# Kernel optimization log

Hardware: AMD Instinct MI355X
Metric: run time of the kernel (lower is better)

Reference implementation:

```python
import jax, jax.numpy as jnp
import numpy as np
from jax import lax

B, T, D = 64, 1024, 256   # batch, seq_len, input_size
H, C = 1024, 1000         # hidden_size, num_classes


def setup_inputs() -> dict:
    key = jax.random.key(0)
    k_x, k_ih, k_hh, k_b, k_fc, k_fb = jax.random.split(key, 6)
    x = jax.random.normal(k_x, (B, T, D), dtype=jnp.float32)
    # scaled init so the 1024-step recurrence stays numerically sane
    w_ih = jax.random.normal(k_ih, (H, D), dtype=jnp.float32) * (1.0 / np.sqrt(D))
    w_hh = jax.random.normal(k_hh, (H, H), dtype=jnp.float32) * (0.5 / np.sqrt(H))
    b_mod = jax.random.normal(k_b, (H,), dtype=jnp.float32) * 0.01 - 0.1
    w_fc = jax.random.normal(k_fc, (C, H), dtype=jnp.float32) * (1.0 / np.sqrt(H))
    b_fc = jnp.zeros((C,), dtype=jnp.float32)
    return {"x": x, "w_ih": w_ih, "w_hh": w_hh, "b_mod": b_mod,
            "w_fc": w_fc, "b_fc": b_fc}


def reference(x, w_ih, w_hh, b_mod, w_fc, b_fc):
    # modReLU RNN: h_t = sign(z_t) * relu(|z_t| + b),  z_t = W_ih x_t + W_hh h_{t-1}
    # fc head applied to last hidden state (out[:, -1, :]).
    bsz = x.shape[0]
    # precompute input projections for all timesteps: [B, T, H]
    xproj = jnp.einsum('btd,hd->bth', x, w_ih)

    def step(h, x_t):
        z = x_t + h @ w_hh.T                      # [B, H]
        h_new = jnp.sign(z) * jnp.maximum(jnp.abs(z) + b_mod, 0.0)
        return h_new, None

    h0 = jnp.zeros((bsz, w_hh.shape[0]), dtype=x.dtype)
    h_last, _ = lax.scan(step, h0, jnp.swapaxes(xproj, 0, 1))  # scan over T
    return h_last @ w_fc.T + b_fc  # [B, C]
```

## Files before the change

### kernel.cpp

```cpp
#include <hip/hip_runtime.h>

typedef __bf16 bf16;
typedef __bf16 bf16x4 __attribute__((ext_vector_type(4)));
typedef __bf16 bf16x8 __attribute__((ext_vector_type(8)));
typedef float f32x4 __attribute__((ext_vector_type(4)));
typedef int   i32x4 __attribute__((ext_vector_type(4)));
typedef unsigned long long u64;
typedef unsigned int u32;

#define T_STEPS 1024
#define BATCH   64
#define DIN     256
#define HID     1024
#define NBLK    32
#define RING    8
#define SENT    0x7F7F7F7Fu

__global__ __launch_bounds__(256) void xproj_gemm(
    const float* __restrict__ x, const float* __restrict__ w_ih,
    bf16* __restrict__ xproj)
{
    __shared__ bf16 As[128 * 40];
    __shared__ bf16 Bs[128 * 40];
    const int tid = threadIdx.x;
    const int m0 = blockIdx.x * 128;
    const int n0 = blockIdx.y * 128;
    const int w = tid >> 6, lane = tid & 63;
    const int r = lane & 15, q = lane >> 4;

    f32x4 acc[2][8];
    #pragma unroll
    for (int i = 0; i < 2; i++)
        #pragma unroll
        for (int j = 0; j < 8; j++)
            acc[i][j] = (f32x4){0.f, 0.f, 0.f, 0.f};

    for (int kk = 0; kk < 8; kk++) {
        const int k0 = kk * 32;
        __syncthreads();
        #pragma unroll
        for (int j = 0; j < 4; j++) {
            int u = tid + j * 256;
            int row = u >> 3, c4 = u & 7;
            float4 fa = *(const float4*)&x[(size_t)(m0 + row) * DIN + k0 + c4 * 4];
            bf16x4 va = { (bf16)fa.x, (bf16)fa.y, (bf16)fa.z, (bf16)fa.w };
            *(bf16x4*)&As[row * 40 + c4 * 4] = va;
            float4 fb = *(const float4*)&w_ih[(size_t)(n0 + row) * DIN + k0 + c4 * 4];
            bf16x4 vb = { (bf16)fb.x, (bf16)fb.y, (bf16)fb.z, (bf16)fb.w };
            *(bf16x4*)&Bs[row * 40 + c4 * 4] = vb;
        }
        __syncthreads();
        bf16x8 a0 = *(const bf16x8*)&As[(w * 32 + r) * 40 + q * 8];
        bf16x8 a1 = *(const bf16x8*)&As[(w * 32 + 16 + r) * 40 + q * 8];
        #pragma unroll
        for (int nt = 0; nt < 8; nt++) {
            bf16x8 bb = *(const bf16x8*)&Bs[(nt * 16 + r) * 40 + q * 8];
            acc[0][nt] = __builtin_amdgcn_mfma_f32_16x16x32_bf16(a0, bb, acc[0][nt], 0, 0, 0);
            acc[1][nt] = __builtin_amdgcn_mfma_f32_16x16x32_bf16(a1, bb, acc[1][nt], 0, 0, 0);
        }
    }

    #pragma unroll
    for (int mi = 0; mi < 2; mi++)
        #pragma unroll
        for (int nt = 0; nt < 8; nt++)
            #pragma unroll
            for (int reg = 0; reg < 4; reg++) {
                int gm = m0 + w * 32 + mi * 16 + q * 4 + reg;
                int n  = n0 + nt * 16 + r;
                int b  = gm >> 10, t = gm & 1023;
                xproj[(((t << 6) + b) << 10) + n] = (bf16)acc[mi][nt][reg];
            }
}

__global__ __launch_bounds__(512, 2) void rnn_rec(
    const float* __restrict__ w_hh, const float* __restrict__ b_mod,
    const bf16* __restrict__ xproj, u64* __restrict__ hbuf,
    float* __restrict__ hT)
{
    __shared__ bf16 Wl[64 * 1032];
    __shared__ float Red[24 * 272];

    const int tid = threadIdx.x;
    const int fg2 = (int)(blockIdx.x >> 1);
    const int half = (int)(blockIdx.x & 1);
    const int f0 = fg2 * 64;
    const int b0 = half * 32;
    const int w = tid >> 6, lane = tid & 63;
    const int r = lane & 15, q = lane >> 4;
    const int bg = w & 1, kq = w >> 1;
    const int batchA = b0 + bg * 16 + r;

    for (int j = 0; j < 32; j++) {
        int u = tid + j * 512;
        int row = u >> 8, c4 = u & 255;
        float4 f = *(const float4*)&w_hh[(size_t)(f0 + row) * HID + c4 * 4];
        bf16x4 v = { (bf16)f.x, (bf16)f.y, (bf16)f.z, (bf16)f.w };
        *(bf16x4*)&Wl[row * 1032 + c4 * 4] = v;
    }
    const int myF = f0 + kq * 16 + r;
    const float bc = b_mod[myF];
    __syncthreads();

    bf16x8 Bf[4][8];
    #pragma unroll
    for (int nt = 0; nt < 4; nt++)
        #pragma unroll
        for (int ks = 0; ks < 8; ks++)
            Bf[nt][ks] = *(const bf16x8*)&Wl[(nt * 16 + r) * 1032 + kq * 256 + ks * 32 + q * 8];

    u32* hbuf32 = (u32*)hbuf;
    const size_t fragOff = (size_t)batchA * 2048 + kq * 512 + q * 16;

    float xpv[4];
    #pragma unroll
    for (int reg = 0; reg < 4; reg++) {
        int b = b0 + bg * 16 + q * 4 + reg;
        xpv[reg] = (float)xproj[(b << 10) + myF];
    }

    for (int t = 0; t < T_STEPS; t++) {
        const int rp = t & (RING - 1), wp = (t + 1) & (RING - 1);
        const char* Hb = (const char*)hbuf + (size_t)rp * 131072 + fragOff;

        union { i32x4 v[8]; u32 wd[32]; bf16x8 f[8]; } A;
        for (;;) {
            asm volatile(
                "global_load_dwordx4 %0, %8, off sc0 sc1\n\t"
                "global_load_dwordx4 %1, %8, off offset:64 sc0 sc1\n\t"
                "global_load_dwordx4 %2, %8, off offset:128 sc0 sc1\n\t"
                "global_load_dwordx4 %3, %8, off offset:192 sc0 sc1\n\t"
                "global_load_dwordx4 %4, %8, off offset:256 sc0 sc1\n\t"
                "global_load_dwordx4 %5, %8, off offset:320 sc0 sc1\n\t"
                "global_load_dwordx4 %6, %8, off offset:384 sc0 sc1\n\t"
                "global_load_dwordx4 %7, %8, off offset:448 sc0 sc1\n\t"
                "s_waitcnt vmcnt(0)"
                : "=v"(A.v[0]), "=v"(A.v[1]), "=v"(A.v[2]), "=v"(A.v[3]),
                  "=v"(A.v[4]), "=v"(A.v[5]), "=v"(A.v[6]), "=v"(A.v[7])
                : "v"(Hb)
                : "memory");
            bool ok = true;
            #pragma unroll
            for (int i = 0; i < 32; i++) ok &= (A.wd[i] != SENT);
            if (__all((int)ok)) break;
        }

        f32x4 acc[4];
        #pragma unroll
        for (int nt = 0; nt < 4; nt++) acc[nt] = (f32x4){0.f,0.f,0.f,0.f};
        #pragma unroll
        for (int ks = 0; ks < 8; ks++)
            #pragma unroll
            for (int nt = 0; nt < 4; nt++)
                acc[nt] = __builtin_amdgcn_mfma_f32_16x16x32_bf16(A.f[ks], Bf[nt][ks], acc[nt], 0, 0, 0);

        #pragma unroll
        for (int nt = 0; nt < 4; nt++) {
            if (nt == kq) continue;
            const int s = (kq - nt - 1) & 3;
            const int base = ((bg * 4 + nt) * 3 + s) * 272;
            #pragma unroll
            for (int reg = 0; reg < 4; reg++)
                Red[base + (q * 4 + reg) * 17 + r] = acc[nt][reg];
        }
        __syncthreads();

        float hv4[4];
        #pragma unroll
        for (int reg = 0; reg < 4; reg++) {
            float z = acc[kq][reg];
            #pragma unroll
            for (int s = 0; s < 3; s++)
                z += Red[((bg * 4 + kq) * 3 + s) * 272 + (q * 4 + reg) * 17 + r];
            z += xpv[reg];
            hv4[reg] = copysignf(fmaxf(fabsf(z) + bc, 0.0f), z);
        }
        __syncthreads();

        if (t == T_STEPS - 1) {
            #pragma unroll
            for (int reg = 0; reg < 4; reg++)
                hT[myF * 64 + b0 + bg * 16 + q * 4 + reg] = hv4[reg];
        } else {
            #pragma unroll
            for (int reg = 0; reg < 4; reg++) {
                const int b = b0 + bg * 16 + q * 4 + reg;
                float other = __shfl_xor(hv4[reg], 1);
                if ((r & 1) == 0) {
                    u32 lo = (u32)__builtin_bit_cast(unsigned short, (bf16)hv4[reg]);
                    u32 hi = (u32)__builtin_bit_cast(unsigned short, (bf16)other);
                    __hip_atomic_store(&hbuf32[(size_t)wp * 32768 + (b << 9) + (myF >> 1)],
                                       lo | (hi << 16), __ATOMIC_RELAXED, __HIP_MEMORY_SCOPE_AGENT);
                }
            }
            const size_t sp = (size_t)((t + 4) & (RING - 1)) * 32768;
            #pragma unroll
            for (int reg = 0; reg < 4; reg++) {
                const int b = b0 + bg * 16 + q * 4 + reg;
                if ((r & 1) == 0)
                    __hip_atomic_store(&hbuf32[sp + (b << 9) + (myF >> 1)],
                                       SENT, __ATOMIC_RELAXED, __HIP_MEMORY_SCOPE_AGENT);
            }
            #pragma unroll
            for (int reg = 0; reg < 4; reg++) {
                int b = b0 + bg * 16 + q * 4 + reg;
                xpv[reg] = (float)xproj[((size_t)(t + 1) << 16) + (b << 10) + myF];
            }
        }
    }
}

__global__ __launch_bounds__(256) void fc_head(
    const float* __restrict__ hT, const float* __restrict__ w_fc,
    const float* __restrict__ b_fc, float* __restrict__ out)
{
    const int tid = threadIdx.x;
    const int b = tid & 63;
    const int c = blockIdx.x * 4 + (tid >> 6);
    float acc = b_fc[c];
    #pragma unroll 8
    for (int k = 0; k < HID; k++)
        acc = fmaf(hT[k * 64 + b], w_fc[(size_t)c * HID + k], acc);
    out[b * 1000 + c] = acc;
}

extern "C" void kernel_launch(void* const* d_in, const int* in_sizes, int n_in,
                              void* d_out, int out_size, void* d_ws, size_t ws_size,
                              hipStream_t stream)
{
    const float* x     = (const float*)d_in[0];
    const float* w_ih  = (const float*)d_in[1];
    const float* w_hh  = (const float*)d_in[2];
    const float* b_mod = (const float*)d_in[3];
    const float* w_fc  = (const float*)d_in[4];
    const float* b_fc  = (const float*)d_in[5];
    float* out = (float*)d_out;

    char* ws = (char*)d_ws;
    bf16*  xproj = (bf16*)ws;
    u64*   hbuf  = (u64*)(ws + 134217728);
    float* hT    = (float*)(ws + 134217728 + 1048576);

    hipMemsetAsync(hbuf, 0, 131072, stream);
    hipMemsetAsync((char*)hbuf + 131072, 0x7F, 7 * 131072, stream);

    dim3 g1(512, 8);
    xproj_gemm<<<g1, 256, 0, stream>>>(x, w_ih, xproj);
    rnn_rec<<<NBLK, 512, 0, stream>>>(w_hh, b_mod, xproj, hbuf, hT);
    fc_head<<<250, 256, 0, stream>>>(hT, w_fc, b_fc, out);
}
```

Baseline: 5.019 ms.

## Restructure recurrence into 16 blocks with software-pipelined prefetched h polling

The recurrent kernel now runs 16 blocks of 256 threads. Each block owns 64 hidden features and processes all 64 batch rows as four 16-row sub-steps, where the old kernel split each feature group across two blocks by batch half. The hidden-state fragment for the next sub-step is loaded with relaxed atomic loads into a double buffer while the current sub-step computes, so the spin-wait on the ring buffer overlaps with MFMA work. The aim is to hide global-memory poll latency and cut cross-block synchronization. The cost is four serialized sub-steps per timestep in each block, fewer CUs in use, and a __syncthreads per sub-step.

```diff
diff --git a/kernel.cpp b/kernel.cpp
--- a/kernel.cpp
+++ b/kernel.cpp
@@ -4,16 +4,15 @@
 typedef __bf16 bf16x4 __attribute__((ext_vector_type(4)));
 typedef __bf16 bf16x8 __attribute__((ext_vector_type(8)));
 typedef float f32x4 __attribute__((ext_vector_type(4)));
-typedef int   i32x4 __attribute__((ext_vector_type(4)));
 typedef unsigned long long u64;
+typedef u64 u64x2 __attribute__((ext_vector_type(2)));
 typedef unsigned int u32;
 
 #define T_STEPS 1024
 #define BATCH   64
 #define DIN     256
 #define HID     1024
-#define NBLK    32
-#define RING    8
+#define NFB     16
 #define SENT    0x7F7F7F7Fu
 
 __global__ __launch_bounds__(256) void xproj_gemm(
@@ -73,26 +72,46 @@
             }
 }
 
-__global__ __launch_bounds__(512, 2) void rnn_rec(
+__device__ __forceinline__ void poll_issue(u64* dst, const u64* src)
+{
+    #pragma unroll
+    for (int j = 0; j < 8; j++) {
+        dst[2 * j]     = __hip_atomic_load(src + (size_t)j * 8,
+                                           __ATOMIC_RELAXED, __HIP_MEMORY_SCOPE_AGENT);
+        dst[2 * j + 1] = __hip_atomic_load(src + (size_t)j * 8 + 1,
+                                           __ATOMIC_RELAXED, __HIP_MEMORY_SCOPE_AGENT);
+    }
+    __builtin_amdgcn_sched_barrier(0);
+}
+
+__device__ __forceinline__ int poll_clean(const u64* b)
+{
+    int ok = 1;
+    #pragma unroll
+    for (int j = 0; j < 16; j++) {
+        u64 v = b[j];
+        ok &= ((u32)v != SENT);
+        ok &= ((u32)(v >> 32) != SENT);
+    }
+    return __all(ok);
+}
+
+__global__ __launch_bounds__(256, 1) void rnn_rec(
     const float* __restrict__ w_hh, const float* __restrict__ b_mod,
     const bf16* __restrict__ xproj, u64* __restrict__ hbuf,
     float* __restrict__ hT)
 {
     __shared__ bf16 Wl[64 * 1032];
-    __shared__ float Red[24 * 272];
-
-    const int tid = threadIdx.x;
-    const int fg2 = (int)(blockIdx.x >> 1);
-    const int half = (int)(blockIdx.x & 1);
-    const int f0 = fg2 * 64;
-    const int b0 = half * 32;
-    const int w = tid >> 6, lane = tid & 63;
+    __shared__ f32x4 Red[2][12][64];
+
+    const int tid  = threadIdx.x;
+    const int f0   = (int)blockIdx.x * 64;
+    const int kq   = tid >> 6;
+    const int lane = tid & 63;
     const int r = lane & 15, q = lane >> 4;
-    const int bg = w & 1, kq = w >> 1;
-    const int batchA = b0 + bg * 16 + r;
-
-    for (int j = 0; j < 32; j++) {
-        int u = tid + j * 512;
+
+    for (int j = 0; j < 64; j++) {
+        int u = tid + j * 256;
         int row = u >> 8, c4 = u & 255;
         float4 f = *(const float4*)&w_hh[(size_t)(f0 + row) * HID + c4 * 4];
         bf16x4 v = { (bf16)f.x, (bf16)f.y, (bf16)f.z, (bf16)f.w };
@@ -110,101 +129,91 @@
             Bf[nt][ks] = *(const bf16x8*)&Wl[(nt * 16 + r) * 1032 + kq * 256 + ks * 32 + q * 8];
 
     u32* hbuf32 = (u32*)hbuf;
-    const size_t fragOff = (size_t)batchA * 2048 + kq * 512 + q * 16;
-
-    float xpv[4];
-    #pragma unroll
-    for (int reg = 0; reg < 4; reg++) {
-        int b = b0 + bg * 16 + q * 4 + reg;
-        xpv[reg] = (float)xproj[(b << 10) + myF];
-    }
+    const int fragU = r * 256 + kq * 64 + q * 2;
+
+    float xpv[4][4];
+    #pragma unroll
+    for (int s = 0; s < 4; s++)
+        #pragma unroll
+        for (int reg = 0; reg < 4; reg++)
+            xpv[s][reg] = (float)xproj[((s * 16 + q * 4 + reg) << 10) + myF];
+
+    u64 pb[2][16];
+    poll_issue(pb[0], hbuf + 0 * 4096 + fragU);
+    poll_issue(pb[1], hbuf + 1 * 4096 + fragU);
 
     for (int t = 0; t < T_STEPS; t++) {
-        const int rp = t & (RING - 1), wp = (t + 1) & (RING - 1);
-        const char* Hb = (const char*)hbuf + (size_t)rp * 131072 + fragOff;
-
-        union { i32x4 v[8]; u32 wd[32]; bf16x8 f[8]; } A;
-        for (;;) {
-            asm volatile(
-                "global_load_dwordx4 %0, %8, off sc0 sc1\n\t"
-                "global_load_dwordx4 %1, %8, off offset:64 sc0 sc1\n\t"
-                "global_load_dwordx4 %2, %8, off offset:128 sc0 sc1\n\t"
-                "global_load_dwordx4 %3, %8, off offset:192 sc0 sc1\n\t"
-                "global_load_dwordx4 %4, %8, off offset:256 sc0 sc1\n\t"
-                "global_load_dwordx4 %5, %8, off offset:320 sc0 sc1\n\t"
-                "global_load_dwordx4 %6, %8, off offset:384 sc0 sc1\n\t"
-                "global_load_dwordx4 %7, %8, off offset:448 sc0 sc1\n\t"
-                "s_waitcnt vmcnt(0)"
-                : "=v"(A.v[0]), "=v"(A.v[1]), "=v"(A.v[2]), "=v"(A.v[3]),
-                  "=v"(A.v[4]), "=v"(A.v[5]), "=v"(A.v[6]), "=v"(A.v[7])
-                : "v"(Hb)
-                : "memory");
-            bool ok = true;
-            #pragma unroll
-            for (int i = 0; i < 32; i++) ok &= (A.wd[i] != SENT);
-            if (__all((int)ok)) break;
-        }
-
-        f32x4 acc[4];
-        #pragma unroll
-        for (int nt = 0; nt < 4; nt++) acc[nt] = (f32x4){0.f,0.f,0.f,0.f};
-        #pragma unroll
-        for (int ks = 0; ks < 8; ks++)
-            #pragma unroll
-            for (int nt = 0; nt < 4; nt++)
-                acc[nt] = __builtin_amdgcn_mfma_f32_16x16x32_bf16(A.f[ks], Bf[nt][ks], acc[nt], 0, 0, 0);
-
-        #pragma unroll
-        for (int nt = 0; nt < 4; nt++) {
-            if (nt == kq) continue;
-            const int s = (kq - nt - 1) & 3;
-            const int base = ((bg * 4 + nt) * 3 + s) * 272;
-            #pragma unroll
-            for (int reg = 0; reg < 4; reg++)
-                Red[base + (q * 4 + reg) * 17 + r] = acc[nt][reg];
-        }
-        __syncthreads();
-
-        float hv4[4];
-        #pragma unroll
-        for (int reg = 0; reg < 4; reg++) {
-            float z = acc[kq][reg];
-            #pragma unroll
-            for (int s = 0; s < 3; s++)
-                z += Red[((bg * 4 + kq) * 3 + s) * 272 + (q * 4 + reg) * 17 + r];
-            z += xpv[reg];
-            hv4[reg] = copysignf(fmaxf(fabsf(z) + bc, 0.0f), z);
-        }
-        __syncthreads();
-
-        if (t == T_STEPS - 1) {
-            #pragma unroll
-            for (int reg = 0; reg < 4; reg++)
-                hT[myF * 64 + b0 + bg * 16 + q * 4 + reg] = hv4[reg];
-        } else {
+        const int rp = t & 7, wp = (t + 1) & 7, sp = (t + 4) & 7;
+        #pragma unroll
+        for (int s = 0; s < 4; s++) {
+            const int par = s & 1;
+
+            if (!poll_clean(pb[par])) {
+                const u64* src = hbuf + (size_t)rp * 16384 + s * 4096 + fragU;
+                do { poll_issue(pb[par], src); } while (!poll_clean(pb[par]));
+            }
+
+            f32x4 acc[4];
+            #pragma unroll
+            for (int nt = 0; nt < 4; nt++) acc[nt] = (f32x4){0.f, 0.f, 0.f, 0.f};
+            #pragma unroll
+            for (int ks = 0; ks < 8; ks++) {
+                u64x2 w2 = { pb[par][2 * ks], pb[par][2 * ks + 1] };
+                bf16x8 af = __builtin_bit_cast(bf16x8, w2);
+                #pragma unroll
+                for (int nt = 0; nt < 4; nt++)
+                    acc[nt] = __builtin_amdgcn_mfma_f32_16x16x32_bf16(af, Bf[nt][ks], acc[nt], 0, 0, 0);
+            }
+
+            {
+                const int s2 = (s + 2) & 3;
+                const int t2 = t + (s >> 1);
+                if (t2 < T_STEPS) {
+                    const int rp2 = t2 & 7;
+                    poll_issue(pb[par], hbuf + (size_t)rp2 * 16384 + s2 * 4096 + fragU);
+                }
+            }
+
+            #pragma unroll
+            for (int nt = 0; nt < 4; nt++) {
+                if (nt == kq) continue;
+                const int sidx = (kq - nt - 1) & 3;
+                Red[par][nt * 3 + sidx][lane] = acc[nt];
+            }
+            __syncthreads();
+
+            f32x4 z4 = acc[kq];
+            #pragma unroll
+            for (int si = 0; si < 3; si++) z4 += Red[par][kq * 3 + si][lane];
+            float hv4[4];
             #pragma unroll
             for (int reg = 0; reg < 4; reg++) {
-                const int b = b0 + bg * 16 + q * 4 + reg;
-                float other = __shfl_xor(hv4[reg], 1);
-                if ((r & 1) == 0) {
-                    u32 lo = (u32)__builtin_bit_cast(unsigned short, (bf16)hv4[reg]);
-                    u32 hi = (u32)__builtin_bit_cast(unsigned short, (bf16)other);
-                    __hip_atomic_store(&hbuf32[(size_t)wp * 32768 + (b << 9) + (myF >> 1)],
-                                       lo | (hi << 16), __ATOMIC_RELAXED, __HIP_MEMORY_SCOPE_AGENT);
+                float z = z4[reg] + xpv[s][reg];
+                hv4[reg] = copysignf(fmaxf(fabsf(z) + bc, 0.0f), z);
+            }
+
+            if (t == T_STEPS - 1) {
+                float4 o; o.x = hv4[0]; o.y = hv4[1]; o.z = hv4[2]; o.w = hv4[3];
+                *(float4*)&hT[myF * 64 + s * 16 + q * 4] = o;
+            } else {
+                #pragma unroll
+                for (int reg = 0; reg < 4; reg++) {
+                    const int b = s * 16 + q * 4 + reg;
+                    float other = __shfl_xor(hv4[reg], 1);
+                    if ((r & 1) == 0) {
+                        u32 lo = (u32)__builtin_bit_cast(unsigned short, (bf16)hv4[reg]);
+                        u32 hi = (u32)__builtin_bit_cast(unsigned short, (bf16)other);
+                        __hip_atomic_store(&hbuf32[(size_t)wp * 32768 + b * 512 + (myF >> 1)],
+                                           lo | (hi << 16), __ATOMIC_RELAXED, __HIP_MEMORY_SCOPE_AGENT);
+                        __hip_atomic_store(&hbuf32[(size_t)sp * 32768 + b * 512 + (myF >> 1)],
+                                           SENT, __ATOMIC_RELAXED, __HIP_MEMORY_SCOPE_AGENT);
+                    }
                 }
-            }
-            const size_t sp = (size_t)((t + 4) & (RING - 1)) * 32768;
-            #pragma unroll
-            for (int reg = 0; reg < 4; reg++) {
-                const int b = b0 + bg * 16 + q * 4 + reg;
-                if ((r & 1) == 0)
-                    __hip_atomic_store(&hbuf32[sp + (b << 9) + (myF >> 1)],
-                                       SENT, __ATOMIC_RELAXED, __HIP_MEMORY_SCOPE_AGENT);
-            }
-            #pragma unroll
-            for (int reg = 0; reg < 4; reg++) {
-                int b = b0 + bg * 16 + q * 4 + reg;
-                xpv[reg] = (float)xproj[((size_t)(t + 1) << 16) + (b << 10) + myF];
+                #pragma unroll
+                for (int reg = 0; reg < 4; reg++) {
+                    const int b = s * 16 + q * 4 + reg;
+                    xpv[s][reg] = (float)xproj[((size_t)(t + 1) << 16) + (b << 10) + myF];
+                }
             }
         }
     }
@@ -246,6 +255,6 @@
 
     dim3 g1(512, 8);
     xproj_gemm<<<g1, 256, 0, stream>>>(x, w_ih, xproj);
-    rnn_rec<<<NBLK, 512, 0, stream>>>(w_hh, b_mod, xproj, hbuf, hT);
+    rnn_rec<<<NFB, 256, 0, stream>>>(w_hh, b_mod, xproj, hbuf, hT);
     fc_head<<<250, 256, 0, stream>>>(hT, w_fc, b_fc, out);
 }
```

Result: slower. 12.66 ms (+152.3%).
